# Optimization experiments

Hardware: AMD Instinct MI355X
Metric: run time of the kernel (lower is better)

Reference implementation:

```python
import jax, jax.numpy as jnp
import numpy as np

N_NODES = 100000
N_EDGES = 1600000
N_RELS = 19
DIMS = [1, 128, 128, 64]  # in_degree feature -> dims


def setup_inputs() -> dict:
    key = jax.random.key(0)
    ks = jax.random.split(key, 12)
    src = jax.random.randint(ks[0], (N_EDGES,), 0, N_NODES, dtype=jnp.int64)
    dst = jax.random.randint(ks[1], (N_EDGES,), 0, N_NODES, dtype=jnp.int64)
    etypes = jax.random.randint(ks[2], (N_EDGES,), 0, N_RELS, dtype=jnp.int64)
    inp = {"src": src, "dst": dst, "etypes": etypes}
    for i, (din, dout) in enumerate(zip(DIMS[:-1], DIMS[1:])):
        s = 1.0 / np.sqrt(max(din, 1))
        inp[f"W{i}"] = jax.random.normal(ks[3 + 3 * i], (N_RELS, din, dout), jnp.float32) * s
        inp[f"Wloop{i}"] = jax.random.normal(ks[4 + 3 * i], (din, dout), jnp.float32) * s
        inp[f"b{i}"] = jnp.zeros((dout,), jnp.float32)
    inp["num_nodes"] = N_NODES
    return inp


def _rel_graph_conv(h, src, dst, etypes, W, Wloop, b, num_nodes, activation):
    # per-relation transform of every node: [N, R, dout]
    transformed = jnp.einsum('nd,rdo->nro', h, W)
    # gather message per edge by (src node, edge relation): [E, dout]
    msg = transformed[src, etypes]
    # scatter-sum to destination nodes
    agg = jax.ops.segment_sum(msg, dst, num_segments=num_nodes)
    out = agg + h @ Wloop + b
    if activation is not None:
        out = activation(out)
    return out


def reference(src, dst, etypes, W0, Wloop0, b0, W1, Wloop1, b1, W2, Wloop2, b2, num_nodes):
    # h = g.in_degrees().view(-1, 1).float()
    deg = jax.ops.segment_sum(jnp.ones_like(dst, dtype=jnp.float32), dst,
                              num_segments=num_nodes)
    h = deg[:, None]
    h = _rel_graph_conv(h, src, dst, etypes, W0, Wloop0, b0, num_nodes, jax.nn.relu)
    h = _rel_graph_conv(h, src, dst, etypes, W1, Wloop1, b1, num_nodes, jax.nn.relu)
    h = _rel_graph_conv(h, src, dst, etypes, W2, Wloop2, b2, num_nodes, None)
    return h
```

## Files before the change

### kernel.cpp

```cpp
#include <hip/hip_runtime.h>
#include <hip/hip_bf16.h>
#include <stdint.h>

#define N_NODES 100000
#define N_EDGES 1600000
#define N_RELS  19
#define NQ      4
#define QN      25000
#define QTILES  196
#define NBQ     98
#define NSB     (NQ * NBQ)
#define N_BUCK  (NQ * N_RELS)
#define NBIN    391
#define NGR     8
#define NBK8    (N_BUCK * NGR)
#define NBIN8   (NBIN * NGR)
#define NHC     (N_BUCK + NBIN)
#define NHC2    (2 * NHC)
#define MSGQ    460000
#define NCKQ    3700
#define NCK_TOT 14000
#define EPB     2048
#define S1B     782

typedef __attribute__((ext_vector_type(8))) short bf16x8;
typedef __attribute__((ext_vector_type(4))) float f32x4;
typedef __attribute__((ext_vector_type(4))) int   int4v;

__device__ __forceinline__ unsigned short f2bf(float x) {
  union { float f; unsigned u; } v; v.f = x;
  unsigned r = v.u + 0x7FFF + ((v.u >> 16) & 1);
  return (unsigned short)(r >> 16);
}
__device__ __forceinline__ float bf2f(unsigned short b) {
  union { unsigned u; float f; } v; v.u = ((unsigned)b) << 16; return v.f;
}

__global__ void k_prep_w(const float* W1, const float* W2,
                         const float* Wl1, const float* Wl2,
                         unsigned short* Wt1, unsigned short* Wt2,
                         unsigned short* Wtl1, unsigned short* Wtl2) {
  int i = blockIdx.x * 256 + threadIdx.x;
  const int s1 = N_RELS * 128 * 128;
  const int s2 = N_RELS * 64 * 128;
  const int s3 = 128 * 128;
  const int s4 = 64 * 128;
  if (i < s1) {
    int r = i / (128 * 128); int rem = i % (128 * 128);
    int n = rem / 128, k = rem % 128;
    Wt1[i] = f2bf(W1[((size_t)r * 128 + k) * 128 + n]);
  } else if (i < s1 + s2) {
    int j = i - s1;
    int r = j / (64 * 128); int rem = j % (64 * 128);
    int n = rem / 128, k = rem % 128;
    Wt2[j] = f2bf(W2[((size_t)r * 128 + k) * 64 + n]);
  } else if (i < s1 + s2 + s3) {
    int j = i - s1 - s2; int n = j / 128, k = j % 128;
    Wtl1[j] = f2bf(Wl1[k * 128 + n]);
  } else if (i < s1 + s2 + s3 + s4) {
    int j = i - s1 - s2 - s3; int n = j / 128, k = j % 128;
    Wtl2[j] = f2bf(Wl2[k * 64 + n]);
  }
}

__global__ void k_hist(const int* __restrict__ dst, const int* __restrict__ et,
                       int* __restrict__ bcount8, int* __restrict__ bincount8,
                       int* __restrict__ histAll) {
  __shared__ int hK[N_BUCK], hB[NBIN];
  __shared__ int sb[256];
  int t = threadIdx.x, g = blockIdx.x & (NGR - 1);
  for (int i = t; i < N_BUCK; i += 256) hK[i] = 0;
  for (int i = t; i < NBIN; i += 256) hB[i] = 0;
  __syncthreads();
  int e0 = blockIdx.x * EPB;
  for (int r = 0; r < EPB / 256; r++) {
    int e = e0 + r * 256 + t;
    if (e < N_EDGES) {
      int d = dst[e];
      atomicAdd(&hK[(d / QN) * N_RELS + et[e]], 1);
      atomicAdd(&hB[d >> 8], 1);
    }
  }
  __syncthreads();
  int* hout = histAll + (size_t)blockIdx.x * NHC2;
  for (int i = t; i < N_BUCK; i += 256) {
    hout[i] = hK[i];
    if (hK[i]) atomicAdd(&bcount8[i * NGR + g], hK[i]);
  }
  for (int i = t; i < NBIN; i += 256) {
    hout[N_BUCK + i] = hB[i];
    if (hB[i]) atomicAdd(&bincount8[i * NGR + g], hB[i]);
  }
  {
    int v0 = (2 * t < N_BUCK) ? hK[2 * t] : 0;
    int v1 = (2 * t + 1 < N_BUCK) ? hK[2 * t + 1] : 0;
    sb[t] = v0 + v1;
    __syncthreads();
    for (int s = 1; s < 256; s <<= 1) {
      int x = (t >= s) ? sb[t - s] : 0;
      __syncthreads();
      sb[t] += x;
      __syncthreads();
    }
    int base = sb[t] - v0 - v1;
    if (2 * t < N_BUCK) hout[NHC + 2 * t] = base;
    if (2 * t + 1 < N_BUCK) hout[NHC + 2 * t + 1] = base + v0;
    __syncthreads();
  }
  {
    int v0 = (2 * t < NBIN) ? hB[2 * t] : 0;
    int v1 = (2 * t + 1 < NBIN) ? hB[2 * t + 1] : 0;
    sb[t] = v0 + v1;
    __syncthreads();
    for (int s = 1; s < 256; s <<= 1) {
      int x = (t >= s) ? sb[t - s] : 0;
      __syncthreads();
      sb[t] += x;
      __syncthreads();
    }
    int base = sb[t] - v0 - v1;
    if (2 * t < NBIN) hout[NHC + N_BUCK + 2 * t] = base;
    if (2 * t + 1 < NBIN) hout[NHC + N_BUCK + 2 * t + 1] = base + v0;
  }
}

__global__ void k_scan0(const int* __restrict__ bcount8, const int* __restrict__ bincount8,
                        int* boff, int* bcur8, int* cbase, int* qcs, int* selfb,
                        int* binoff8, int* bincur8) {
  __shared__ int shK[NBK8];
  __shared__ int sb76[N_BUCK];
  __shared__ int sbs[N_BUCK];
  __shared__ int sh[512];
  int t = threadIdx.x;
  for (int i = t; i < NBK8; i += 512) shK[i] = bcount8[i];
  __syncthreads();
  if (t < N_BUCK) {
    int s = 0;
    for (int gg = 0; gg < NGR; gg++) s += shK[t * NGR + gg];
    sb76[t] = s;
  }
  __syncthreads();
  if (t == 0) {
    int a = 0, cb = 0;
    for (int q = 0; q < NQ; q++) {
      qcs[q] = cb;
      for (int r = 0; r < N_RELS; r++) {
        int b = q * N_RELS + r;
        boff[b] = a; sbs[b] = a; cbase[b] = cb;
        a += sb76[b]; cb += (sb76[b] + 127) >> 7;
      }
      selfb[q] = cb; cb += QTILES;
    }
    qcs[NQ] = cb;
    boff[N_BUCK] = a;
  }
  __syncthreads();
  for (int i = t; i < NBK8; i += 512) {
    int b = i >> 3, gg = i & (NGR - 1);
    int base = sbs[b];
    for (int k = 0; k < gg; k++) base += shK[b * NGR + k];
    bcur8[i] = base;
  }
  int vals[7];
  int i0 = t * 7;
  int loc = 0;
  for (int k = 0; k < 7; k++) {
    int i = i0 + k;
    int v = (i < NBIN8) ? bincount8[i] : 0;
    vals[k] = v; loc += v;
  }
  sh[t] = loc;
  __syncthreads();
  for (int s = 1; s < 512; s <<= 1) {
    int x = (t >= s) ? sh[t - s] : 0;
    __syncthreads();
    sh[t] += x;
    __syncthreads();
  }
  int run = sh[t] - loc;
  for (int k = 0; k < 7; k++) {
    int i = i0 + k;
    if (i < NBIN8) { binoff8[i] = run; bincur8[i] = run; run += vals[k]; }
  }
  if (t == 511) binoff8[NBIN8] = sh[511];
}

__launch_bounds__(256)
__global__ void k_scat1a(const int* __restrict__ src, const int* __restrict__ dst,
                         const int* __restrict__ et,
                         const int* __restrict__ histAll,
                         int* __restrict__ bcur8,
                         int* __restrict__ srcS, int* __restrict__ posE) {
  __shared__ int sortK[EPB];
  __shared__ int lK[N_BUCK], gKr[N_BUCK];
  int t = threadIdx.x, blk = blockIdx.x, g = blk & (NGR - 1);
  const int* hin = histAll + (size_t)blk * NHC2;
  for (int i = t; i < N_BUCK; i += 256) {
    int h = hin[i], l = hin[NHC + i];
    lK[i] = l;
    gKr[i] = h ? (atomicAdd(&bcur8[i * NGR + g], h) - l) : 0;
  }
  __syncthreads();
  int e0 = blk * EPB;
  int nval = min(EPB, N_EDGES - e0);
  for (int r = 0; r < EPB / 256; r++) {
    int e = e0 + r * 256 + t;
    if (e < N_EDGES) {
      int d = dst[e], rl = et[e], sv = src[e];
      int bk = (d / QN) * N_RELS + rl;
      int lrk = atomicAdd(&lK[bk], 1);
      sortK[lrk] = sv | (bk << 17);
      posE[e] = gKr[bk] + lrk;
    }
  }
  __syncthreads();
  for (int r = 0; r < EPB / 256; r++) {
    int s = r * 256 + t;
    if (s < nval) {
      int v = sortK[s];
      srcS[gKr[v >> 17] + s] = v & 0x1FFFF;
    }
  }
}

__launch_bounds__(256)
__global__ void k_scat1b(const int* __restrict__ src, const int* __restrict__ dst,
                         const int* __restrict__ et,
                         const int* __restrict__ posE,
                         const int* __restrict__ histAll,
                         int* __restrict__ bincur8,
                         int* __restrict__ stgA, int* __restrict__ stgB) {
  __shared__ int sortA[EPB], sortBv[EPB];
  __shared__ int lB[NBIN], gBr[NBIN];
  int t = threadIdx.x, blk = blockIdx.x, g = blk & (NGR - 1);
  const int* hin = histAll + (size_t)blk * NHC2;
  for (int i = t; i < NBIN; i += 256) {
    int h = hin[N_BUCK + i], l = hin[NHC + N_BUCK + i];
    lB[i] = l;
    gBr[i] = h ? (atomicAdd(&bincur8[i * NGR + g], h) - l) : 0;
  }
  __syncthreads();
  int e0 = blk * EPB;
  int nval = min(EPB, N_EDGES - e0);
  for (int r = 0; r < EPB / 256; r++) {
    int e = e0 + r * 256 + t;
    if (e < N_EDGES) {
      int d = dst[e], rl = et[e], sv = src[e];
      int gpos = posE[e];
      int bn = d >> 8;
      int lrb = atomicAdd(&lB[bn], 1);
      sortA[lrb] = gpos | (rl << 21) | ((bn & 63) << 26);
      sortBv[lrb] = sv | ((d & 255) << 17) | ((bn >> 6) << 25);
    }
  }
  __syncthreads();
  for (int r = 0; r < EPB / 256; r++) {
    int s = r * 256 + t;
    if (s < nval) {
      int a = sortA[s], b = sortBv[s];
      int bn = ((a >> 26) & 63) | (((b >> 25) & 7) << 6);
      int adr = gBr[bn] + s;
      stgA[adr] = a & 0x03FFFFFF;
      stgB[adr] = b & 0x01FFFFFF;
    }
  }
}

__global__ void k_cnt(const int* __restrict__ stgB, const int* __restrict__ binoff8,
                      int* __restrict__ ncount) {
  __shared__ int c[256];
  int b = blockIdx.x, t = threadIdx.x;
  c[t] = 0;
  __syncthreads();
  int lo = binoff8[b * NGR], hi = binoff8[b * NGR + NGR];
  for (int s = lo + t; s < hi; s += 256)
    atomicAdd(&c[(stgB[s] >> 17) & 255], 1);
  __syncthreads();
  int n = b * 256 + t;
  if (n < N_NODES) ncount[n] = c[t];
}

__global__ void k_scanA(const int* __restrict__ ncount, int* __restrict__ bsum) {
  __shared__ int sh[256];
  int b = blockIdx.x, t = threadIdx.x;
  int q = b / NBQ, bb = b % NBQ;
  int i = bb * 256 + t;
  int val = (i < QN) ? (ncount[q * QN + i] + 1) : 0;
  sh[t] = val;
  __syncthreads();
  for (int s = 128; s > 0; s >>= 1) {
    if (t < s) sh[t] += sh[t + s];
    __syncthreads();
  }
  if (t == 0) bsum[b] = sh[0];
}

__global__ void k_scanB(const int* bsum, int* bbase, int* nodeoff) {
  __shared__ int sh[NSB];
  int t = threadIdx.x;
  if (t < NSB) sh[t] = bsum[t];
  __syncthreads();
  if (t < NQ) {
    int a = 0;
    for (int i = 0; i < NBQ; i++) {
      int v = sh[t * NBQ + i]; sh[t * NBQ + i] = a; a += v;
    }
    nodeoff[(t + 1) * QN + t] = a;
  }
  __syncthreads();
  if (t < NSB) bbase[t] = sh[t];
}

__global__ void k_scanC(const int* __restrict__ ncount,
                        const int* __restrict__ bbase,
                        const int* __restrict__ boff,
                        int* __restrict__ nodeoff, int* __restrict__ ginv) {
  __shared__ int sh[256];
  int b = blockIdx.x, t = threadIdx.x;
  int q = b / NBQ, bb = b % NBQ;
  int i = bb * 256 + t;
  int val = (i < QN) ? (ncount[q * QN + i] + 1) : 0;
  sh[t] = val;
  __syncthreads();
  for (int s = 1; s < 256; s <<= 1) {
    int x = (t >= s) ? sh[t - s] : 0;
    __syncthreads();
    sh[t] += x;
    __syncthreads();
  }
  int excl = sh[t] - val + bbase[b];
  if (i < QN) {
    int n = q * QN + i;
    nodeoff[n + q] = excl;
    int qedges = boff[(q + 1) * N_RELS] - boff[q * N_RELS];
    ginv[(size_t)q * MSGQ + excl] = qedges + i;
  }
}

__global__ void k_scat2(const int* __restrict__ stgA, const int* __restrict__ stgB,
                        const int* __restrict__ binoff8,
                        const int* __restrict__ nodeoff,
                        const int* __restrict__ ncount,
                        const int* __restrict__ boff,
                        int* __restrict__ ginv, int* __restrict__ msgS) {
  __shared__ int cur[256];
  __shared__ int qe0s[NQ + 1];
  int b = blockIdx.x, t = threadIdx.x;
  if (t <= NQ) qe0s[t] = boff[t * N_RELS];
  int n = b * 256 + t;
  if (n < N_NODES) {
    int q = n / QN;
    cur[t] = nodeoff[n + q] + 1;
  }
  __syncthreads();
  int lo = binoff8[b * NGR], hi = binoff8[b * NGR + NGR];
  for (int s = lo + t; s < hi; s += 256) {
    int a = stgA[s], bb = stgB[s];
    int dlow = (bb >> 17) & 255;
    int slot = atomicAdd(&cur[dlow], 1);
    int pos = a & 0x1FFFFF, rel = (a >> 21) & 31;
    int sv = bb & 0x1FFFF;
    int d = b * 256 + dlow;
    int q = d / QN;
    size_t qb = (size_t)q * MSGQ;
    ginv[qb + slot] = pos - qe0s[q];
    msgS[qb + slot] = (ncount[sv] << 5) | rel;
  }
}

__global__ void k_fill(const int* boff, const int* cbase,
                       const int* selfb, int* cA, int* cB) {
  int b = blockIdx.x;
  if (b < N_BUCK) {
    int cnt = boff[b + 1] - boff[b], e0 = boff[b], w0 = cbase[b];
    int rel = b % N_RELS;
    int nch = (cnt + 127) >> 7;
    for (int i = threadIdx.x; i < nch; i += blockDim.x) {
      cA[w0 + i] = (e0 + i * 128) | (rel << 21);
      cB[w0 + i] = min(128, cnt - i * 128);
    }
  } else {
    int q = b - N_BUCK;
    int w0 = selfb[q];
    for (int i = threadIdx.x; i < QTILES; i += blockDim.x) {
      cA[w0 + i] = (i * 128) | (19 << 21);
      cB[w0 + i] = min(128, QN - i * 128);
    }
  }
}

__global__ void k_reduce0(const int* __restrict__ msgS,
                          const int* __restrict__ nodeoff,
                          const int* __restrict__ ncount,
                          const float* __restrict__ W0,
                          const float* __restrict__ Wl0,
                          const float* __restrict__ b0,
                          unsigned short* __restrict__ h1) {
  __shared__ float W0s[N_RELS * 128];
  __shared__ float wl[128], bb[128];
  int t = threadIdx.x;
  for (int i = t; i < N_RELS * 128; i += 256) W0s[i] = W0[i];
  if (t < 128) { wl[t] = Wl0[t]; bb[t] = b0[t]; }
  __syncthreads();
  int n = blockIdx.x * 8 + (t >> 5);
  if (n >= N_NODES) return;
  int q = n / QN;
  int l = t & 31;
  int lo = nodeoff[n + q], hi = nodeoff[n + q + 1];
  const int* ms = msgS + (size_t)q * MSGQ;
  float dn = (float)ncount[n];
  int c0 = l * 4;
  float a0 = dn * wl[c0]     + bb[c0];
  float a1 = dn * wl[c0 + 1] + bb[c0 + 1];
  float a2 = dn * wl[c0 + 2] + bb[c0 + 2];
  float a3 = dn * wl[c0 + 3] + bb[c0 + 3];
  for (int i = lo + 1; i < hi; i++) {
    int w = ms[i];
    float dg = (float)(w >> 5);
    const float* wr = &W0s[(w & 31) * 128 + c0];
    a0 += dg * wr[0]; a1 += dg * wr[1];
    a2 += dg * wr[2]; a3 += dg * wr[3];
  }
  a0 = fmaxf(a0, 0.f); a1 = fmaxf(a1, 0.f);
  a2 = fmaxf(a2, 0.f); a3 = fmaxf(a3, 0.f);
  uint2 o;
  o.x = (unsigned)f2bf(a0) | ((unsigned)f2bf(a1) << 16);
  o.y = (unsigned)f2bf(a2) | ((unsigned)f2bf(a3) << 16);
  *(uint2*)&h1[(size_t)n * 128 + c0] = o;
}

template <int NOUT>
__launch_bounds__(256, NOUT == 64 ? 6 : 4)
__global__ void k_gemm_msg(const unsigned short* __restrict__ hprev,
                           const unsigned short* __restrict__ Wt,
                           const unsigned short* __restrict__ Wtl,
                           const int* __restrict__ qcs, int q,
                           const int* __restrict__ cA,
                           const int* __restrict__ cB,
                           const int* __restrict__ srcS,
                           const int* __restrict__ boff,
                           unsigned short* __restrict__ msg) {
  const int LDK = 136;
  __shared__ __align__(16) unsigned short Bs[NOUT * LDK];

  int cs = qcs[q], ce = qcs[q + 1];
  int w = blockIdx.x;
  if (w >= ce - cs) return;
  w += cs;
  int pa = cA[w];
  int e0 = pa & 0x1FFFFF, rel = pa >> 21;
  int cnt = cB[w];
  bool self = (rel == 19);
  const unsigned short* wsrc = self ? Wtl : (Wt + (size_t)rel * NOUT * 128);
  int qe0 = boff[q * N_RELS];
  int qedges = boff[(q + 1) * N_RELS] - qe0;
  int ppos0 = self ? (qedges + e0) : (e0 - qe0);
  int tid = threadIdx.x;
  const int lane = tid & 63, wid = tid >> 6;

  int rowg[2]; bool valv[2];
#pragma unroll
  for (int fi = 0; fi < 2; fi++) {
    int m = wid * 32 + fi * 16 + (lane & 15);
    bool v = m < cnt;
    valv[fi] = v;
    int row = 0;
    if (v) row = self ? (q * QN + e0 + m) : srcS[e0 + m];
    rowg[fi] = row;
  }
  bf16x8 a[2][4];
#pragma unroll
  for (int fi = 0; fi < 2; fi++) {
    const unsigned short* rp = hprev + (size_t)rowg[fi] * 128 + (lane >> 4) * 8;
#pragma unroll
    for (int kk = 0; kk < 4; kk++)
      a[fi][kk] = *(const bf16x8*)&rp[kk * 32];
  }
#pragma unroll
  for (int fi = 0; fi < 2; fi++)
    if (!valv[fi]) {
#pragma unroll
      for (int kk = 0; kk < 4; kk++)
        a[fi][kk] = (bf16x8){0, 0, 0, 0, 0, 0, 0, 0};
    }

  for (int task = tid; task < NOUT * 16; task += 256) {
    int n = task >> 4, c = task & 15;
    *(int4v*)&Bs[n * LDK + c * 8] = *(const int4v*)&wsrc[n * 128 + c * 8];
  }
  __syncthreads();

  const int FJ = NOUT / 16;
  f32x4 acc[2][FJ];
#pragma unroll
  for (int i = 0; i < 2; i++)
#pragma unroll
    for (int j = 0; j < FJ; j++) acc[i][j] = (f32x4){0.f, 0.f, 0.f, 0.f};

#pragma unroll
  for (int kk = 0; kk < 4; kk++) {
    int kof = kk * 32 + (lane >> 4) * 8;
    bf16x8 b[FJ];
#pragma unroll
    for (int fj = 0; fj < FJ; fj++)
      b[fj] = *(const bf16x8*)&Bs[(fj * 16 + (lane & 15)) * LDK + kof];
#pragma unroll
    for (int fi = 0; fi < 2; fi++)
#pragma unroll
      for (int fj = 0; fj < FJ; fj++)
        acc[fi][fj] = __builtin_amdgcn_mfma_f32_16x16x32_bf16(a[fi][kk], b[fj], acc[fi][fj], 0, 0, 0);
  }

  __syncthreads();
  unsigned short* Cs = Bs;
#pragma unroll
  for (int fi = 0; fi < 2; fi++)
#pragma unroll
    for (int fj = 0; fj < FJ; fj++)
#pragma unroll
      for (int j = 0; j < 4; j++) {
        int mrow = wid * 32 + fi * 16 + (lane >> 4) * 4 + j;
        int col = fj * 16 + (lane & 15);
        Cs[mrow * NOUT + col] = f2bf(acc[fi][fj][j]);
      }
  __syncthreads();
  const int CW = NOUT / 8;
  for (int task = tid; task < cnt * CW; task += 256) {
    int row = task / CW, c = task % CW;
    *(int4v*)&msg[(size_t)(ppos0 + row) * NOUT + c * 8] =
        *(const int4v*)&Cs[row * NOUT + c * 8];
  }
}

template <int NOUT>
__global__ void k_reduce(const unsigned short* __restrict__ msg,
                         const int* __restrict__ ginv,
                         const int* __restrict__ nodeoff, int q,
                         const float* __restrict__ bias, int do_relu,
                         unsigned short* __restrict__ outh,
                         float* __restrict__ outf) {
  int t = threadIdx.x;
  int rn = blockIdx.x * 8 + (t >> 5);
  if (rn >= QN) return;
  int n = q * QN + rn;
  int l = t & 31;
  int lo = nodeoff[n + q], hi = nodeoff[n + q + 1];
  const int* gv = ginv + (size_t)q * MSGQ;
  if (NOUT == 128) {
    float a0 = 0.f, a1 = 0.f, a2 = 0.f, a3 = 0.f;
    for (int i = lo; i < hi; i++) {
      int ppos = gv[i];
      uint2 v = *(const uint2*)&msg[(size_t)ppos * 128 + l * 4];
      a0 += bf2f((unsigned short)(v.x & 0xffff));
      a1 += bf2f((unsigned short)(v.x >> 16));
      a2 += bf2f((unsigned short)(v.y & 0xffff));
      a3 += bf2f((unsigned short)(v.y >> 16));
    }
    a0 += bias[l * 4];     a1 += bias[l * 4 + 1];
    a2 += bias[l * 4 + 2]; a3 += bias[l * 4 + 3];
    if (do_relu) {
      a0 = fmaxf(a0, 0.f); a1 = fmaxf(a1, 0.f);
      a2 = fmaxf(a2, 0.f); a3 = fmaxf(a3, 0.f);
    }
    uint2 o;
    o.x = (unsigned)f2bf(a0) | ((unsigned)f2bf(a1) << 16);
    o.y = (unsigned)f2bf(a2) | ((unsigned)f2bf(a3) << 16);
    *(uint2*)&outh[(size_t)n * 128 + l * 4] = o;
  } else {
    float a0 = 0.f, a1 = 0.f;
    for (int i = lo; i < hi; i++) {
      int ppos = gv[i];
      unsigned v = *(const unsigned*)&msg[(size_t)ppos * 64 + l * 2];
      a0 += bf2f((unsigned short)(v & 0xffff));
      a1 += bf2f((unsigned short)(v >> 16));
    }
    a0 += bias[l * 2];
    a1 += bias[l * 2 + 1];
    if (do_relu) { a0 = fmaxf(a0, 0.f); a1 = fmaxf(a1, 0.f); }
    outf[(size_t)n * 64 + l * 2]     = a0;
    outf[(size_t)n * 64 + l * 2 + 1] = a1;
  }
}

extern "C" void kernel_launch(void* const* d_in, const int* in_sizes, int n_in,
                              void* d_out, int out_size, void* d_ws, size_t ws_size,
                              hipStream_t stream) {
  const int* src = (const int*)d_in[0];
  const int* dst = (const int*)d_in[1];
  const int* et  = (const int*)d_in[2];
  const float* W0  = (const float*)d_in[3];
  const float* Wl0 = (const float*)d_in[4];
  const float* b0  = (const float*)d_in[5];
  const float* W1  = (const float*)d_in[6];
  const float* Wl1 = (const float*)d_in[7];
  const float* b1  = (const float*)d_in[8];
  const float* W2  = (const float*)d_in[9];
  const float* Wl2 = (const float*)d_in[10];
  const float* b2  = (const float*)d_in[11];

  char* ws = (char*)d_ws;
  size_t off = 0;
  auto alloc = [&](size_t bytes) {
    void* p = ws + off;
    off = (off + bytes + 255) & ~(size_t)255;
    return p;
  };
  unsigned short* msg = (unsigned short*)alloc((size_t)MSGQ * 128 * 2);
  unsigned short* h1 = (unsigned short*)alloc((size_t)N_NODES * 128 * 2);
  unsigned short* h2 = (unsigned short*)alloc((size_t)N_NODES * 128 * 2);
  int* srcS = (int*)alloc((size_t)N_EDGES * 4);
  int* stgA = (int*)alloc((size_t)N_EDGES * 4);
  int* stgB = (int*)alloc((size_t)N_EDGES * 4);
  int* posE = (int*)alloc((size_t)N_EDGES * 4);
  int* msgS = (int*)alloc((size_t)NQ * MSGQ * 4);
  int* ginv = (int*)alloc((size_t)NQ * MSGQ * 4);
  int* ncount  = (int*)alloc((size_t)N_NODES * 4);
  int* nodeoff = (int*)alloc((size_t)(N_NODES + NQ + 4) * 4);
  int* histAll = (int*)alloc((size_t)S1B * NHC2 * 4);
  unsigned short* Wt1  = (unsigned short*)alloc((size_t)N_RELS * 128 * 128 * 2);
  unsigned short* Wt2  = (unsigned short*)alloc((size_t)N_RELS * 64 * 128 * 2);
  unsigned short* Wtl1 = (unsigned short*)alloc((size_t)128 * 128 * 2);
  unsigned short* Wtl2 = (unsigned short*)alloc((size_t)64 * 128 * 2);
  int* acc0 = (int*)alloc((size_t)(NBK8 + NBIN8) * 4);
  int* bcount8   = acc0;
  int* bincount8 = acc0 + NBK8;
  int* ints = (int*)alloc(4096);
  int* boff   = ints;
  int* cbase  = ints + 80;
  int* qcs    = ints + 160;
  int* selfb  = ints + 168;
  int* bcur8  = (int*)alloc((size_t)NBK8 * 4);
  int* binoff8 = (int*)alloc((size_t)(NBIN8 + 1) * 4);
  int* bincur8 = (int*)alloc((size_t)NBIN8 * 4);
  int* bsum  = (int*)alloc((size_t)NSB * 4);
  int* bbase = (int*)alloc((size_t)NSB * 4);
  int* cA = (int*)alloc((size_t)NCK_TOT * 4);
  int* cB = (int*)alloc((size_t)NCK_TOT * 4);

  hipMemsetAsync(acc0, 0, (size_t)(NBK8 + NBIN8) * 4, stream);

  k_prep_w<<<1920, 256, 0, stream>>>(W1, W2, Wl1, Wl2, Wt1, Wt2, Wtl1, Wtl2);
  k_hist<<<S1B, 256, 0, stream>>>(dst, et, bcount8, bincount8, histAll);
  k_scan0<<<1, 512, 0, stream>>>(bcount8, bincount8, boff, bcur8, cbase, qcs,
                                 selfb, binoff8, bincur8);
  k_scat1a<<<S1B, 256, 0, stream>>>(src, dst, et, histAll, bcur8, srcS, posE);
  k_scat1b<<<S1B, 256, 0, stream>>>(src, dst, et, posE, histAll, bincur8,
                                    stgA, stgB);
  k_cnt<<<NBIN, 256, 0, stream>>>(stgB, binoff8, ncount);
  k_scanA<<<NSB, 256, 0, stream>>>(ncount, bsum);
  k_scanB<<<1, 512, 0, stream>>>(bsum, bbase, nodeoff);
  k_scanC<<<NSB, 256, 0, stream>>>(ncount, bbase, boff, nodeoff, ginv);
  k_scat2<<<NBIN, 256, 0, stream>>>(stgA, stgB, binoff8, nodeoff, ncount, boff,
                                    ginv, msgS);
  k_fill<<<N_BUCK + NQ, 256, 0, stream>>>(boff, cbase, selfb, cA, cB);
  k_reduce0<<<(N_NODES + 7) / 8, 256, 0, stream>>>(msgS, nodeoff, ncount,
                                                   W0, Wl0, b0, h1);

  for (int q = 0; q < NQ; q++) {
    k_gemm_msg<128><<<NCKQ, 256, 0, stream>>>(h1, Wt1, Wtl1, qcs, q, cA, cB,
                                              srcS, boff, msg);
    k_reduce<128><<<QN / 8, 256, 0, stream>>>(msg, ginv, nodeoff, q, b1, 1,
                                              h2, nullptr);
  }
  for (int q = 0; q < NQ; q++) {
    k_gemm_msg<64><<<NCKQ, 256, 0, stream>>>(h2, Wt2, Wtl2, qcs, q, cA, cB,
                                             srcS, boff, msg);
    k_reduce<64><<<QN / 8, 256, 0, stream>>>(msg, ginv, nodeoff, q, b2, 0,
                                             nullptr, (float*)d_out);
  }
}
```

Before: 729.6 us.

## Replace layer-0 per-edge reduction with per-node relation-degree histogram in shared memory

Layer 0 has scalar input features, so the aggregated message equals the sum over relations of (sum of source degrees for that relation) times the W0 row. A new kernel builds a per-destination, per-relation sum in shared memory using atomics over the binned edges, then does a small 19x128 matvec per node. This removes the msgS array, its scatter writes in k_scat2, and the per-edge loop in k_reduce0. The trade-off is about 19 KB of LDS for the histogram, lower occupancy, and one thread per node doing all 128 outputs with strided shared reads.

```diff
diff --git a/kernel.cpp b/kernel.cpp
--- a/kernel.cpp
+++ b/kernel.cpp
@@ -340,9 +340,8 @@
 __global__ void k_scat2(const int* __restrict__ stgA, const int* __restrict__ stgB,
                         const int* __restrict__ binoff8,
                         const int* __restrict__ nodeoff,
-                        const int* __restrict__ ncount,
                         const int* __restrict__ boff,
-                        int* __restrict__ ginv, int* __restrict__ msgS) {
+                        int* __restrict__ ginv) {
   __shared__ int cur[256];
   __shared__ int qe0s[NQ + 1];
   int b = blockIdx.x, t = threadIdx.x;
@@ -358,13 +357,62 @@
     int a = stgA[s], bb = stgB[s];
     int dlow = (bb >> 17) & 255;
     int slot = atomicAdd(&cur[dlow], 1);
-    int pos = a & 0x1FFFFF, rel = (a >> 21) & 31;
-    int sv = bb & 0x1FFFF;
+    int pos = a & 0x1FFFFF;
     int d = b * 256 + dlow;
     int q = d / QN;
-    size_t qb = (size_t)q * MSGQ;
-    ginv[qb + slot] = pos - qe0s[q];
-    msgS[qb + slot] = (ncount[sv] << 5) | rel;
+    ginv[(size_t)q * MSGQ + slot] = pos - qe0s[q];
+  }
+}
+
+__global__ void k_rsum(const int* __restrict__ stgA, const int* __restrict__ stgB,
+                       const int* __restrict__ binoff8,
+                       const int* __restrict__ ncount,
+                       const float* __restrict__ W0,
+                       const float* __restrict__ Wl0,
+                       const float* __restrict__ b0,
+                       unsigned short* __restrict__ h1) {
+  __shared__ int R[256][N_RELS];
+  __shared__ float W0s[N_RELS * 128];
+  __shared__ float wl[128], bb[128];
+  int b = blockIdx.x, t = threadIdx.x;
+  for (int i = t; i < N_RELS * 128; i += 256) W0s[i] = W0[i];
+  if (t < 128) { wl[t] = Wl0[t]; bb[t] = b0[t]; }
+#pragma unroll
+  for (int r = 0; r < N_RELS; r++) R[t][r] = 0;
+  __syncthreads();
+  int lo = binoff8[b * NGR], hi = binoff8[b * NGR + NGR];
+  for (int s = lo + t; s < hi; s += 256) {
+    int a = stgA[s], bv = stgB[s];
+    int rel = (a >> 21) & 31;
+    int sv = bv & 0x1FFFF;
+    int dlow = (bv >> 17) & 255;
+    atomicAdd(&R[dlow][rel], ncount[sv]);
+  }
+  __syncthreads();
+  int n = b * 256 + t;
+  if (n >= N_NODES) return;
+  float rr[N_RELS];
+#pragma unroll
+  for (int r = 0; r < N_RELS; r++) rr[r] = (float)R[t][r];
+  float dn = (float)ncount[n];
+  unsigned short* hp = &h1[(size_t)n * 128];
+  for (int c0 = 0; c0 < 128; c0 += 8) {
+    float acc[8];
+#pragma unroll
+    for (int j = 0; j < 8; j++) acc[j] = dn * wl[c0 + j] + bb[c0 + j];
+    for (int r = 0; r < N_RELS; r++) {
+#pragma unroll
+      for (int j = 0; j < 8; j++)
+        acc[j] += rr[r] * W0s[r * 128 + c0 + j];
+    }
+    unsigned vs[4];
+#pragma unroll
+    for (int j = 0; j < 4; j++) {
+      float x0 = fmaxf(acc[2 * j], 0.f), x1 = fmaxf(acc[2 * j + 1], 0.f);
+      vs[j] = (unsigned)f2bf(x0) | ((unsigned)f2bf(x1) << 16);
+    }
+    int4v o = {(int)vs[0], (int)vs[1], (int)vs[2], (int)vs[3]};
+    *(int4v*)&hp[c0] = o;
   }
 }
 
@@ -387,46 +435,6 @@
       cB[w0 + i] = min(128, QN - i * 128);
     }
   }
-}
-
-__global__ void k_reduce0(const int* __restrict__ msgS,
-                          const int* __restrict__ nodeoff,
-                          const int* __restrict__ ncount,
-                          const float* __restrict__ W0,
-                          const float* __restrict__ Wl0,
-                          const float* __restrict__ b0,
-                          unsigned short* __restrict__ h1) {
-  __shared__ float W0s[N_RELS * 128];
-  __shared__ float wl[128], bb[128];
-  int t = threadIdx.x;
-  for (int i = t; i < N_RELS * 128; i += 256) W0s[i] = W0[i];
-  if (t < 128) { wl[t] = Wl0[t]; bb[t] = b0[t]; }
-  __syncthreads();
-  int n = blockIdx.x * 8 + (t >> 5);
-  if (n >= N_NODES) return;
-  int q = n / QN;
-  int l = t & 31;
-  int lo = nodeoff[n + q], hi = nodeoff[n + q + 1];
-  const int* ms = msgS + (size_t)q * MSGQ;
-  float dn = (float)ncount[n];
-  int c0 = l * 4;
-  float a0 = dn * wl[c0]     + bb[c0];
-  float a1 = dn * wl[c0 + 1] + bb[c0 + 1];
-  float a2 = dn * wl[c0 + 2] + bb[c0 + 2];
-  float a3 = dn * wl[c0 + 3] + bb[c0 + 3];
-  for (int i = lo + 1; i < hi; i++) {
-    int w = ms[i];
-    float dg = (float)(w >> 5);
-    const float* wr = &W0s[(w & 31) * 128 + c0];
-    a0 += dg * wr[0]; a1 += dg * wr[1];
-    a2 += dg * wr[2]; a3 += dg * wr[3];
-  }
-  a0 = fmaxf(a0, 0.f); a1 = fmaxf(a1, 0.f);
-  a2 = fmaxf(a2, 0.f); a3 = fmaxf(a3, 0.f);
-  uint2 o;
-  o.x = (unsigned)f2bf(a0) | ((unsigned)f2bf(a1) << 16);
-  o.y = (unsigned)f2bf(a2) | ((unsigned)f2bf(a3) << 16);
-  *(uint2*)&h1[(size_t)n * 128 + c0] = o;
 }
 
 template <int NOUT>
@@ -612,7 +620,6 @@
   int* stgA = (int*)alloc((size_t)N_EDGES * 4);
   int* stgB = (int*)alloc((size_t)N_EDGES * 4);
   int* posE = (int*)alloc((size_t)N_EDGES * 4);
-  int* msgS = (int*)alloc((size_t)NQ * MSGQ * 4);
   int* ginv = (int*)alloc((size_t)NQ * MSGQ * 4);
   int* ncount  = (int*)alloc((size_t)N_NODES * 4);
   int* nodeoff = (int*)alloc((size_t)(N_NODES + NQ + 4) * 4);
@@ -650,11 +657,10 @@
   k_scanA<<<NSB, 256, 0, stream>>>(ncount, bsum);
   k_scanB<<<1, 512, 0, stream>>>(bsum, bbase, nodeoff);
   k_scanC<<<NSB, 256, 0, stream>>>(ncount, bbase, boff, nodeoff, ginv);
-  k_scat2<<<NBIN, 256, 0, stream>>>(stgA, stgB, binoff8, nodeoff, ncount, boff,
-                                    ginv, msgS);
+  k_scat2<<<NBIN, 256, 0, stream>>>(stgA, stgB, binoff8, nodeoff, boff, ginv);
   k_fill<<<N_BUCK + NQ, 256, 0, stream>>>(boff, cbase, selfb, cA, cB);
-  k_reduce0<<<(N_NODES + 7) / 8, 256, 0, stream>>>(msgS, nodeoff, ncount,
-                                                   W0, Wl0, b0, h1);
+  k_rsum<<<NBIN, 256, 0, stream>>>(stgA, stgB, binoff8, ncount,
+                                   W0, Wl0, b0, h1);
 
   for (int q = 0; q < NQ; q++) {
     k_gemm_msg<128><<<NCKQ, 256, 0, stream>>>(h1, Wt1, Wtl1, qcs, q, cA, cB,
```

Result: faster. 711.3 us (-2.5%).
